# Kernel tuning notes

Hardware: AMD Instinct MI355X
Metric: run time of the kernel (lower is better)

## Reference

```python
import jax, jax.numpy as jnp
import numpy as np

DIM = 192
WINDOW = 8
HEADS = 6
N = WINDOW * WINDOW


def _relative_position_index(ws):
    coords = np.stack(np.meshgrid(np.arange(ws), np.arange(ws), indexing='ij'))  # (2, ws, ws)
    flat = coords.reshape(2, -1)  # (2, N)
    rel = flat[:, :, None] - flat[:, None, :]  # (2, N, N)
    rel = rel.transpose(1, 2, 0).copy()
    rel[:, :, 0] += ws - 1
    rel[:, :, 1] += ws - 1
    rel[:, :, 0] *= 2 * ws - 1
    return rel.sum(-1).astype(np.int32)  # (N, N)


def setup_inputs() -> dict:
    key = jax.random.key(0)
    ks = jax.random.split(key, 5)
    B_ = 4096
    x = jax.random.normal(ks[0], (B_, N, DIM), dtype=jnp.float32)
    qkv_w = jax.random.normal(ks[1], (3 * DIM, DIM), dtype=jnp.float32) * 0.02
    qkv_b = jnp.zeros((3 * DIM,), dtype=jnp.float32)
    proj_w = jax.random.normal(ks[2], (DIM, DIM), dtype=jnp.float32) * 0.02
    proj_b = jnp.zeros((DIM,), dtype=jnp.float32)
    rpb_table = jax.random.normal(ks[3], ((2 * WINDOW - 1) ** 2, HEADS), dtype=jnp.float32) * 0.02
    rel_idx = jnp.asarray(_relative_position_index(WINDOW))
    return {"x": x, "qkv_w": qkv_w, "qkv_b": qkv_b, "proj_w": proj_w,
            "proj_b": proj_b, "rpb_table": rpb_table, "rel_idx": rel_idx}


def reference(x, qkv_w, qkv_b, proj_w, proj_b, rpb_table, rel_idx):
    B_, n, C = x.shape
    d = C // HEADS
    scale = d ** -0.5
    qkv = x @ qkv_w.T + qkv_b                      # (B_, N, 3C)
    qkv = qkv.reshape(B_, n, 3, HEADS, d).transpose(2, 0, 3, 1, 4)  # (3, B_, H, N, d)
    q, k, v = qkv[0], qkv[1], qkv[2]
    attn = jnp.einsum('bhnd,bhmd->bhnm', q * scale, k)  # (B_, H, N, N)
    bias = rpb_table[rel_idx.reshape(-1)].reshape(n, n, HEADS).transpose(2, 0, 1)  # (H, N, N)
    attn = jax.nn.softmax(attn + bias[None], axis=-1)
    out = jnp.einsum('bhnm,bhmd->bnhd', attn, v).reshape(B_, n, C)
    return out @ proj_w.T + proj_b
```

## Files before the change

kernel.cpp:

```cpp
#include <hip/hip_runtime.h>


constexpr int NT = 64, DIMC = 192, NH = 6;
constexpr float SC = 0.17677669529663687f;

typedef short          s8v __attribute__((ext_vector_type(8)));
typedef float          f4v __attribute__((ext_vector_type(4)));
typedef unsigned short u4v __attribute__((ext_vector_type(4)));

constexpr size_t WS_QKVW  = 0;
constexpr size_t WS_PROJW = WS_QKVW + (size_t)36*6*2*1024;
constexpr size_t WS_BIAS  = WS_PROJW + (size_t)12*6*2*1024;
constexpr size_t WS_QKVB  = WS_BIAS + (size_t)6*4*4*64*16;
constexpr size_t WS_NEED  = WS_QKVB + (size_t)576*4;

__device__ __forceinline__ unsigned short bhi(float x) {
  return (unsigned short)(__builtin_bit_cast(unsigned int, x) >> 16);
}
__device__ __forceinline__ float bft(unsigned short h) {
  return __builtin_bit_cast(float, ((unsigned int)h) << 16);
}
__device__ __forceinline__ unsigned short brne(float x) {
  unsigned int u = __builtin_bit_cast(unsigned int, x);
  u += 0x7FFFu + ((u >> 16) & 1u);
  return (unsigned short)(u >> 16);
}

#define MFMA16(a, b, c) __builtin_amdgcn_mfma_f32_16x16x32_bf16((a), (b), (c), 0, 0, 0)

__device__ __forceinline__ s8v ld_frag(const unsigned short* base, int idx) {
  u4v a = *(const u4v*)(base + idx);
  u4v b = *(const u4v*)(base + idx + 16);
  s8v r;
  #pragma unroll
  for (int i = 0; i < 4; ++i) { r[i] = (short)a[i]; r[4 + i] = (short)b[i]; }
  return r;
}

__global__ __launch_bounds__(256) void prep_kernel(
    const float* __restrict__ qkv_w, const float* __restrict__ qkv_b,
    const float* __restrict__ proj_w, const float* __restrict__ rpb,
    const int* __restrict__ ridx, char* __restrict__ ws)
{
  const int t = blockIdx.x * 256 + threadIdx.x;
  if (t < 13824) {
    const int lane = t & 63, rest = t >> 6;
    const int kk = rest % 6, nt = rest / 6;
    const int g = lane >> 4, c = lane & 15;
    const int n = 16 * nt + c;
    const float sc = (nt < 12) ? SC : 1.f;
    const float* p = qkv_w + n * 192 + kk * 32 + 4 * g;
    f4v a = *(const f4v*)p;       a *= sc;
    f4v b = *(const f4v*)(p + 16); b *= sc;
    s8v hi, lo;
    #pragma unroll
    for (int i = 0; i < 4; ++i) {
      unsigned short h0 = bhi(a[i]); hi[i]     = (short)h0; lo[i]     = (short)brne(a[i] - bft(h0));
      unsigned short h1 = bhi(b[i]); hi[4 + i] = (short)h1; lo[4 + i] = (short)brne(b[i] - bft(h1));
    }
    s8v* base = (s8v*)(ws + WS_QKVW);
    base[((nt * 6 + kk) * 2 + 0) * 64 + lane] = hi;
    base[((nt * 6 + kk) * 2 + 1) * 64 + lane] = lo;
  } else if (t < 18432) {
    const int t2 = t - 13824;
    const int lane = t2 & 63, rest = t2 >> 6;
    const int h = rest % 6, nt = rest / 6;
    const int g = lane >> 4, c = lane & 15;
    const int n = 16 * nt + c;
    const float* p = proj_w + n * 192 + 32 * h + 4 * g;
    f4v a = *(const f4v*)p;
    f4v b = *(const f4v*)(p + 16);
    s8v hi, lo;
    #pragma unroll
    for (int i = 0; i < 4; ++i) {
      unsigned short h0 = bhi(a[i]); hi[i]     = (short)h0; lo[i]     = (short)brne(a[i] - bft(h0));
      unsigned short h1 = bhi(b[i]); hi[4 + i] = (short)h1; lo[4 + i] = (short)brne(b[i] - bft(h1));
    }
    s8v* base = (s8v*)(ws + WS_PROJW);
    base[((nt * 6 + h) * 2 + 0) * 64 + lane] = hi;
    base[((nt * 6 + h) * 2 + 1) * 64 + lane] = lo;
  } else if (t < 24576) {
    const int t2 = t - 18432;
    const int lane = t2 & 63, rest = t2 >> 6;
    const int nt = rest & 3, mt = (rest >> 2) & 3, h = rest >> 4;
    const int g = lane >> 4, c = lane & 15;
    const int q = 16 * nt + c;
    const int kb = 16 * mt + 4 * g;
    const int* ip = ridx + q * 64 + kb;
    f4v o;
    #pragma unroll
    for (int r = 0; r < 4; ++r) o[r] = rpb[ip[r] * 6 + h];
    ((f4v*)(ws + WS_BIAS))[((h * 4 + mt) * 4 + nt) * 64 + lane] = o;
  } else if (t < 25152) {
    const int i = t - 24576;
    ((float*)(ws + WS_QKVB))[i] = qkv_b[i] * (i < 192 ? SC : 1.f);
  }
}

__global__ __launch_bounds__(256, 2)
void win_attn_mfma(const float* __restrict__ x, const float* __restrict__ proj_b,
                   const char* __restrict__ ws, float* __restrict__ out)
{
  __shared__ alignas(16) unsigned short Qh[64 * 36], Ql[64 * 36];
  __shared__ alignas(16) unsigned short Kh[64 * 36], Kl[64 * 36];
  __shared__ alignas(16) unsigned short Vh[32 * 68], Vl[32 * 68];

  const int tid = threadIdx.x;
  const int wv = tid >> 6, lane = tid & 63, g = lane >> 4, c = lane & 15;
  const size_t win = blockIdx.x;
  const float* xw   = x   + win * (size_t)(NT * DIMC);
  float*       outw = out + win * (size_t)(NT * DIMC);

  const s8v*   qkvw  = (const s8v*)(ws + WS_QKVW);
  const s8v*   projw = (const s8v*)(ws + WS_PROJW);
  const f4v*   biasf = (const f4v*)(ws + WS_BIAS);
  const float* qkvb  = (const float*)(ws + WS_QKVB);

  f4v pacc[12];
  #pragma unroll
  for (int i = 0; i < 12; ++i)
    #pragma unroll
    for (int r = 0; r < 4; ++r) pacc[i][r] = 0.f;

  const float* xbase = xw + (size_t)(16 * wv + c) * DIMC + 4 * g;

  #pragma unroll 1
  for (int h = 0; h < NH; ++h) {
    f4v acc[6];
    #pragma unroll
    for (int j = 0; j < 6; ++j)
      #pragma unroll
      for (int r = 0; r < 4; ++r) acc[j][r] = 0.f;

    #pragma unroll
    for (int kk = 0; kk < 6; ++kk) {
      f4v xa = *(const f4v*)(xbase + 32 * kk);
      f4v xb = *(const f4v*)(xbase + 32 * kk + 16);
      s8v ah, al;
      #pragma unroll
      for (int i = 0; i < 4; ++i) {
        unsigned short h0 = bhi(xa[i]); ah[i]     = (short)h0; al[i]     = (short)brne(xa[i] - bft(h0));
        unsigned short h1 = bhi(xb[i]); ah[4 + i] = (short)h1; al[4 + i] = (short)brne(xb[i] - bft(h1));
      }
      #pragma unroll
      for (int sgj = 0; sgj < 6; ++sgj) {
        const int seg = sgj >> 1, j = sgj & 1;
        const int n576 = seg * 12 + 2 * h + j;
        const s8v bh = qkvw[((n576 * 6 + kk) * 2 + 0) * 64 + lane];
        const s8v bl = qkvw[((n576 * 6 + kk) * 2 + 1) * 64 + lane];
        acc[sgj] = MFMA16(ah, bh, acc[sgj]);
        acc[sgj] = MFMA16(ah, bl, acc[sgj]);
        acc[sgj] = MFMA16(al, bh, acc[sgj]);
      }
    }
    #pragma unroll
    for (int sgj = 0; sgj < 6; ++sgj) {
      const int seg = sgj >> 1, j = sgj & 1;
      const float bv = qkvb[seg * 192 + 32 * h + 16 * j + c];
      if (seg < 2) {
        unsigned short* dh = (seg == 0) ? Qh : Kh;
        unsigned short* dl = (seg == 0) ? Ql : Kl;
        #pragma unroll
        for (int r = 0; r < 4; ++r) {
          const float v = acc[sgj][r] + bv;
          const unsigned short hh = bhi(v);
          dh[(16 * wv + 4 * g + r) * 36 + 16 * j + c] = hh;
          dl[(16 * wv + 4 * g + r) * 36 + 16 * j + c] = brne(v - bft(hh));
        }
      } else {
        u4v hh, ll;
        #pragma unroll
        for (int r = 0; r < 4; ++r) {
          const float v = acc[sgj][r] + bv;
          const unsigned short x0 = bhi(v);
          hh[r] = x0; ll[r] = brne(v - bft(x0));
        }
        *(u4v*)&Vh[(16 * j + c) * 68 + 16 * wv + 4 * g] = hh;
        *(u4v*)&Vl[(16 * j + c) * 68 + 16 * wv + 4 * g] = ll;
      }
    }
    __syncthreads();

    f4v sacc[4];
    #pragma unroll
    for (int mt = 0; mt < 4; ++mt)
      sacc[mt] = biasf[((h * 4 + mt) * 4 + wv) * 64 + lane];

    s8v qbh, qbl;
    {
      const int idx = (16 * wv + c) * 36 + 4 * g;
      qbh = ld_frag(Qh, idx);
      qbl = ld_frag(Ql, idx);
    }
    #pragma unroll
    for (int mt = 0; mt < 4; ++mt) {
      const int idx = (16 * mt + c) * 36 + 4 * g;
      const s8v kh = ld_frag(Kh, idx);
      const s8v kl = ld_frag(Kl, idx);
      sacc[mt] = MFMA16(kh, qbh, sacc[mt]);
      sacc[mt] = MFMA16(kh, qbl, sacc[mt]);
      sacc[mt] = MFMA16(kl, qbh, sacc[mt]);
    }
    float mx = sacc[0][0];
    #pragma unroll
    for (int mt = 0; mt < 4; ++mt)
      #pragma unroll
      for (int r = 0; r < 4; ++r) mx = fmaxf(mx, sacc[mt][r]);
    mx = fmaxf(mx, __shfl_xor(mx, 16));
    mx = fmaxf(mx, __shfl_xor(mx, 32));
    float sum = 0.f;
    float p[4][4];
    #pragma unroll
    for (int mt = 0; mt < 4; ++mt)
      #pragma unroll
      for (int r = 0; r < 4; ++r) { p[mt][r] = __expf(sacc[mt][r] - mx); sum += p[mt][r]; }
    sum += __shfl_xor(sum, 16);
    sum += __shfl_xor(sum, 32);
    const float inv = 1.f / sum;
    unsigned short ph[4][4], pl[4][4];
    #pragma unroll
    for (int mt = 0; mt < 4; ++mt)
      #pragma unroll
      for (int r = 0; r < 4; ++r) {
        const float v = p[mt][r] * inv;
        const unsigned short h0 = bhi(v);
        ph[mt][r] = h0; pl[mt][r] = brne(v - bft(h0));
      }

    f4v oa0, oa1;
    #pragma unroll
    for (int r = 0; r < 4; ++r) { oa0[r] = 0.f; oa1[r] = 0.f; }
    #pragma unroll
    for (int kk = 0; kk < 2; ++kk) {
      s8v pbh, pbl;
      #pragma unroll
      for (int i = 0; i < 4; ++i) {
        pbh[i] = (short)ph[2 * kk][i];     pbl[i] = (short)pl[2 * kk][i];
        pbh[4 + i] = (short)ph[2 * kk + 1][i]; pbl[4 + i] = (short)pl[2 * kk + 1][i];
      }
      #pragma unroll
      for (int mo = 0; mo < 2; ++mo) {
        const int idx = (16 * mo + c) * 68 + 32 * kk + 4 * g;
        const s8v vh = ld_frag(Vh, idx);
        const s8v vl = ld_frag(Vl, idx);
        f4v& o = (mo == 0) ? oa0 : oa1;
        o = MFMA16(vh, pbh, o);
        o = MFMA16(vh, pbl, o);
        o = MFMA16(vl, pbh, o);
      }
    }
    __syncthreads();

    s8v oh, ol;
    #pragma unroll
    for (int i = 0; i < 4; ++i) {
      const unsigned short h0 = bhi(oa0[i]);
      oh[i] = (short)h0; ol[i] = (short)brne(oa0[i] - bft(h0));
      const unsigned short h1 = bhi(oa1[i]);
      oh[4 + i] = (short)h1; ol[4 + i] = (short)brne(oa1[i] - bft(h1));
    }
    #pragma unroll
    for (int nt = 0; nt < 12; ++nt) {
      const s8v wh = projw[((nt * 6 + h) * 2 + 0) * 64 + lane];
      const s8v wl = projw[((nt * 6 + h) * 2 + 1) * 64 + lane];
      pacc[nt] = MFMA16(oh, wh, pacc[nt]);
      pacc[nt] = MFMA16(oh, wl, pacc[nt]);
      pacc[nt] = MFMA16(ol, wh, pacc[nt]);
    }
  }

  #pragma unroll
  for (int nt = 0; nt < 12; ++nt) {
    const float pb = proj_b[16 * nt + c];
    #pragma unroll
    for (int r = 0; r < 4; ++r)
      outw[(size_t)(16 * wv + 4 * g + r) * DIMC + 16 * nt + c] = pacc[nt][r] + pb;
  }
}

__global__ __launch_bounds__(256, 2)
void win_attn_kernel(const float* __restrict__ x, const float* __restrict__ qkv_w,
                     const float* __restrict__ qkv_b, const float* __restrict__ proj_w,
                     const float* __restrict__ proj_b, const float* __restrict__ rpb,
                     const int* __restrict__ ridx, float* __restrict__ out)
{
  __shared__ float reg1[32 * 192];
  __shared__ float reg2[48 * 64];
  __shared__ float qs[64 * 36];
  __shared__ float ks[64 * 36];
  __shared__ float vs[64 * 36];

  const int tid = threadIdx.x;
  const int w = blockIdx.x;
  const float* xw = x + (size_t)w * (NT * DIMC);
  float* outw = out + (size_t)w * (NT * DIMC);

  const int cg = tid >> 4;
  const int tgA = tid & 15;
  const int tB = tid >> 2;
  const int jB = tid & 3;
  const int ogD = tid >> 4;
  const int tgD = tid & 15;

  int idxv[16];
  #pragma unroll
  for (int mm = 0; mm < 16; ++mm) idxv[mm] = ridx[tB * 64 + jB + 4 * mm] * NH;

  float oacc[4][12];
  #pragma unroll
  for (int tt = 0; tt < 4; ++tt)
    #pragma unroll
    for (int oo = 0; oo < 12; ++oo) oacc[tt][oo] = 0.f;

  for (int h = 0; h < NH; ++h) {
    float acc[6][4];
    #pragma unroll
    for (int cc = 0; cc < 6; ++cc)
      #pragma unroll
      for (int tt = 0; tt < 4; ++tt) acc[cc][tt] = 0.f;

    for (int i0 = 0; i0 < DIMC; i0 += 48) {
      __syncthreads();
      #pragma unroll
      for (int k = 0; k < 12; ++k) {
        int flat = k * 256 + tid;
        int t = flat & 63, ii = flat >> 6;
        reg2[ii * 64 + t] = xw[t * DIMC + i0 + ii];
      }
      #pragma unroll
      for (int k = 0; k < 18; ++k) {
        int flat = k * 256 + tid;
        int rr = flat % 96, ii = flat / 96;
        int seg = rr >> 5, lc = rr & 31;
        int grow = seg * 192 + h * 32 + lc;
        reg1[ii * 96 + rr] = qkv_w[grow * DIMC + i0 + ii];
      }
      __syncthreads();
      #pragma unroll 2
      for (int i = 0; i < 48; ++i) {
        float4 x4 = *(const float4*)(&reg2[i * 64 + 4 * tgA]);
        const float* wr = &reg1[i * 96 + 6 * cg];
        float2 w0 = *(const float2*)(wr + 0);
        float2 w1 = *(const float2*)(wr + 2);
        float2 w2 = *(const float2*)(wr + 4);
        float xa[4] = {x4.x, x4.y, x4.z, x4.w};
        float wa[6] = {w0.x, w0.y, w1.x, w1.y, w2.x, w2.y};
        #pragma unroll
        for (int cc = 0; cc < 6; ++cc)
          #pragma unroll
          for (int tt = 0; tt < 4; ++tt)
            acc[cc][tt] = fmaf(wa[cc], xa[tt], acc[cc][tt]);
      }
    }
    #pragma unroll
    for (int cc = 0; cc < 6; ++cc) {
      int cch = 6 * cg + cc;
      int seg = cch >> 5, lc = cch & 31;
      float bv = qkv_b[seg * 192 + h * 32 + lc];
      if (seg == 0) {
        #pragma unroll
        for (int tt = 0; tt < 4; ++tt)
          qs[(4 * tgA + tt) * 36 + lc] = (acc[cc][tt] + bv) * SC;
      } else if (seg == 1) {
        #pragma unroll
        for (int tt = 0; tt < 4; ++tt)
          ks[(4 * tgA + tt) * 36 + lc] = acc[cc][tt] + bv;
      } else {
        #pragma unroll
        for (int tt = 0; tt < 4; ++tt)
          vs[(4 * tgA + tt) * 36 + lc] = acc[cc][tt] + bv;
      }
    }
    __syncthreads();

    #pragma unroll
    for (int k = 0; k < 24; ++k) {
      int flat = k * 256 + tid;
      int o = flat % 192, ccc = flat / 192;
      reg1[ccc * 192 + o] = proj_w[o * DIMC + h * 32 + ccc];
    }

    float qr[32];
    {
      const float* qrow = &qs[tB * 36];
      #pragma unroll
      for (int d4 = 0; d4 < 8; ++d4) {
        float4 q4 = *(const float4*)(qrow + 4 * d4);
        qr[4*d4+0] = q4.x; qr[4*d4+1] = q4.y; qr[4*d4+2] = q4.z; qr[4*d4+3] = q4.w;
      }
    }
    float sv[16];
    #pragma unroll
    for (int mm = 0; mm < 16; ++mm) {
      const float* krow = &ks[(jB + 4 * mm) * 36];
      float a = rpb[idxv[mm] + h];
      #pragma unroll
      for (int d4 = 0; d4 < 8; ++d4) {
        float4 k4 = *(const float4*)(krow + 4 * d4);
        a = fmaf(qr[4*d4+0], k4.x, a);
        a = fmaf(qr[4*d4+1], k4.y, a);
        a = fmaf(qr[4*d4+2], k4.z, a);
        a = fmaf(qr[4*d4+3], k4.w, a);
      }
      sv[mm] = a;
    }
    float mx = sv[0];
    #pragma unroll
    for (int mm = 1; mm < 16; ++mm) mx = fmaxf(mx, sv[mm]);
    mx = fmaxf(mx, __shfl_xor(mx, 1));
    mx = fmaxf(mx, __shfl_xor(mx, 2));
    float sum = 0.f;
    #pragma unroll
    for (int mm = 0; mm < 16; ++mm) { sv[mm] = __expf(sv[mm] - mx); sum += sv[mm]; }
    sum += __shfl_xor(sum, 1);
    sum += __shfl_xor(sum, 2);
    const float inv = 1.f / sum;

    float part[32];
    #pragma unroll
    for (int dd = 0; dd < 32; ++dd) part[dd] = 0.f;
    #pragma unroll
    for (int mm = 0; mm < 16; ++mm) {
      float pv = sv[mm] * inv;
      const float* vrow = &vs[(jB + 4 * mm) * 36];
      #pragma unroll
      for (int d4 = 0; d4 < 8; ++d4) {
        float4 v4 = *(const float4*)(vrow + 4 * d4);
        part[4*d4+0] = fmaf(pv, v4.x, part[4*d4+0]);
        part[4*d4+1] = fmaf(pv, v4.y, part[4*d4+1]);
        part[4*d4+2] = fmaf(pv, v4.z, part[4*d4+2]);
        part[4*d4+3] = fmaf(pv, v4.w, part[4*d4+3]);
      }
    }
    float p16[16];
    {
      const bool hi2 = (jB & 1);
      #pragma unroll
      for (int k2 = 0; k2 < 16; ++k2) {
        float lo_v = part[k2], hi_v = part[16 + k2];
        float sendv = hi2 ? lo_v : hi_v;
        float keepv = hi2 ? hi_v : lo_v;
        float got = __shfl_xor(sendv, 1);
        p16[k2] = keepv + got;
      }
    }
    float p8[8];
    {
      const bool hi2 = (jB & 2);
      #pragma unroll
      for (int k2 = 0; k2 < 8; ++k2) {
        float lo_v = p16[k2], hi_v = p16[8 + k2];
        float sendv = hi2 ? lo_v : hi_v;
        float keepv = hi2 ? hi_v : lo_v;
        float got = __shfl_xor(sendv, 2);
        p8[k2] = keepv + got;
      }
    }
    const int dd0 = (jB & 1) * 16 + (jB & 2) * 4;
    #pragma unroll
    for (int k2 = 0; k2 < 8; ++k2)
      reg2[(dd0 + k2) * 64 + tB] = p8[k2];

    __syncthreads();

    {
      const int o0 = 12 * ogD, t0 = 4 * tgD;
      #pragma unroll 2
      for (int cc2 = 0; cc2 < 32; ++cc2) {
        float4 a4 = *(const float4*)(&reg2[cc2 * 64 + t0]);
        const float* pr = &reg1[cc2 * 192 + o0];
        float4 b0 = *(const float4*)(pr + 0);
        float4 b1 = *(const float4*)(pr + 4);
        float4 b2 = *(const float4*)(pr + 8);
        float av[4]  = {a4.x, a4.y, a4.z, a4.w};
        float bw[12] = {b0.x, b0.y, b0.z, b0.w, b1.x, b1.y, b1.z, b1.w,
                        b2.x, b2.y, b2.z, b2.w};
        #pragma unroll
        for (int tt = 0; tt < 4; ++tt)
          #pragma unroll
          for (int oo = 0; oo < 12; ++oo)
            oacc[tt][oo] = fmaf(av[tt], bw[oo], oacc[tt][oo]);
      }
    }
  }

  {
    const int o0 = 12 * ogD, t0 = 4 * tgD;
    #pragma unroll
    for (int oo = 0; oo < 12; ++oo) {
      float pb = proj_b[o0 + oo];
      #pragma unroll
      for (int tt = 0; tt < 4; ++tt)
        outw[(size_t)(t0 + tt) * DIMC + o0 + oo] = oacc[tt][oo] + pb;
    }
  }
}

extern "C" void kernel_launch(void* const* d_in, const int* in_sizes, int n_in,
                              void* d_out, int out_size, void* d_ws, size_t ws_size,
                              hipStream_t stream) {
  const float* x      = (const float*)d_in[0];
  const float* qkv_w  = (const float*)d_in[1];
  const float* qkv_b  = (const float*)d_in[2];
  const float* proj_w = (const float*)d_in[3];
  const float* proj_b = (const float*)d_in[4];
  const float* rpb    = (const float*)d_in[5];
  const int*   ridx   = (const int*)d_in[6];
  float* out = (float*)d_out;
  const int B = in_sizes[0] / (NT * DIMC);

  if (d_ws != nullptr && ws_size >= WS_NEED) {
    hipLaunchKernelGGL(prep_kernel, dim3(99), dim3(256), 0, stream,
                       qkv_w, qkv_b, proj_w, rpb, ridx, (char*)d_ws);
    hipLaunchKernelGGL(win_attn_mfma, dim3(B), dim3(256), 0, stream,
                       x, proj_b, (const char*)d_ws, out);
  } else {
    hipLaunchKernelGGL(win_attn_kernel, dim3(B), dim3(256), 0, stream,
                       x, qkv_w, qkv_b, proj_w, proj_b, rpb, ridx, out);
  }
}
```

Before: 1.035 ms.

## Double-buffer per-head QKV in LDS and overlap next head's projection with attention

Restructures the per-head loop into a software pipeline: Q/K/V LDS buffers are doubled, and the QKV projection MFMAs for head h+1 are issued between the QK^T and softmax/PV of head h, with the output projection of head h-1 deferred into the next iteration. This removes one of the two barriers per head and aims to hide MFMA and global-load latency behind softmax work. Softmax normalisation is also moved after PV (scaling the output by 1/sum instead of scaling the probabilities). LDS use doubles and register pressure rises from the extra live accumulators, which may hurt occupancy at the 2-block launch bound.

```diff
diff --git a/kernel.cpp b/kernel.cpp
--- a/kernel.cpp
+++ b/kernel.cpp
@@ -97,13 +97,183 @@
   }
 }
 
+
+__device__ __forceinline__ void qkv_head(int lane, const float* __restrict__ xbase,
+                                         const s8v* __restrict__ qkvw,
+                                         int h, f4v acc[6]) {
+  #pragma unroll
+  for (int j = 0; j < 6; ++j)
+    #pragma unroll
+    for (int r = 0; r < 4; ++r) acc[j][r] = 0.f;
+  #pragma unroll
+  for (int kk = 0; kk < 6; ++kk) {
+    f4v xa = *(const f4v*)(xbase + 32 * kk);
+    f4v xb = *(const f4v*)(xbase + 32 * kk + 16);
+    s8v ah, al;
+    #pragma unroll
+    for (int i = 0; i < 4; ++i) {
+      unsigned short h0 = bhi(xa[i]); ah[i]     = (short)h0; al[i]     = (short)brne(xa[i] - bft(h0));
+      unsigned short h1 = bhi(xb[i]); ah[4 + i] = (short)h1; al[4 + i] = (short)brne(xb[i] - bft(h1));
+    }
+    #pragma unroll
+    for (int sgj = 0; sgj < 6; ++sgj) {
+      const int seg = sgj >> 1, j = sgj & 1;
+      const int n576 = seg * 12 + 2 * h + j;
+      const s8v bh = qkvw[((n576 * 6 + kk) * 2 + 0) * 64 + lane];
+      const s8v bl = qkvw[((n576 * 6 + kk) * 2 + 1) * 64 + lane];
+      acc[sgj] = MFMA16(ah, bh, acc[sgj]);
+      acc[sgj] = MFMA16(ah, bl, acc[sgj]);
+      acc[sgj] = MFMA16(al, bh, acc[sgj]);
+    }
+  }
+}
+
+__device__ __forceinline__ void qkv_stage(int wv, int g, int c,
+    const f4v acc[6], const float* __restrict__ qkvb, int h,
+    unsigned short* Qh_, unsigned short* Ql_,
+    unsigned short* Kh_, unsigned short* Kl_,
+    unsigned short* Vh_, unsigned short* Vl_) {
+  #pragma unroll
+  for (int sgj = 0; sgj < 6; ++sgj) {
+    const int seg = sgj >> 1, j = sgj & 1;
+    const float bv = qkvb[seg * 192 + 32 * h + 16 * j + c];
+    if (seg < 2) {
+      unsigned short* dh = (seg == 0) ? Qh_ : Kh_;
+      unsigned short* dl = (seg == 0) ? Ql_ : Kl_;
+      #pragma unroll
+      for (int r = 0; r < 4; ++r) {
+        const float v = acc[sgj][r] + bv;
+        const unsigned short hh = bhi(v);
+        dh[(16 * wv + 4 * g + r) * 36 + 16 * j + c] = hh;
+        dl[(16 * wv + 4 * g + r) * 36 + 16 * j + c] = brne(v - bft(hh));
+      }
+    } else {
+      u4v hh, ll;
+      #pragma unroll
+      for (int r = 0; r < 4; ++r) {
+        const float v = acc[sgj][r] + bv;
+        const unsigned short x0 = bhi(v);
+        hh[r] = x0; ll[r] = brne(v - bft(x0));
+      }
+      *(u4v*)&Vh_[(16 * j + c) * 68 + 16 * wv + 4 * g] = hh;
+      *(u4v*)&Vl_[(16 * j + c) * 68 + 16 * wv + 4 * g] = ll;
+    }
+  }
+}
+
+__device__ __forceinline__ void proj_acc(int lane, const s8v oh, const s8v ol,
+                                         const s8v* __restrict__ projw, int h,
+                                         f4v pacc[12]) {
+  #pragma unroll
+  for (int nt = 0; nt < 12; ++nt) {
+    const s8v wh = projw[((nt * 6 + h) * 2 + 0) * 64 + lane];
+    const s8v wl = projw[((nt * 6 + h) * 2 + 1) * 64 + lane];
+    pacc[nt] = MFMA16(oh, wh, pacc[nt]);
+    pacc[nt] = MFMA16(oh, wl, pacc[nt]);
+    pacc[nt] = MFMA16(ol, wh, pacc[nt]);
+  }
+}
+
+template<bool DO_NEXT>
+__device__ __forceinline__ void head_iter(
+    int h, int lane, int wv, int g, int c,
+    const float* __restrict__ xbase,
+    const s8v* __restrict__ qkvw, const f4v* __restrict__ biasf,
+    const float* __restrict__ qkvb,
+    const unsigned short* Qhc, const unsigned short* Qlc,
+    const unsigned short* Khc, const unsigned short* Klc,
+    const unsigned short* Vhc, const unsigned short* Vlc,
+    unsigned short* Qhn, unsigned short* Qln,
+    unsigned short* Khn, unsigned short* Kln,
+    unsigned short* Vhn, unsigned short* Vln,
+    s8v& oh, s8v& ol)
+{
+  f4v sacc[4];
+  #pragma unroll
+  for (int mt = 0; mt < 4; ++mt)
+    sacc[mt] = biasf[((h * 4 + mt) * 4 + wv) * 64 + lane];
+  s8v qbh, qbl;
+  {
+    const int idx = (16 * wv + c) * 36 + 4 * g;
+    qbh = ld_frag(Qhc, idx);
+    qbl = ld_frag(Qlc, idx);
+  }
+  #pragma unroll
+  for (int mt = 0; mt < 4; ++mt) {
+    const int idx = (16 * mt + c) * 36 + 4 * g;
+    const s8v kh = ld_frag(Khc, idx);
+    const s8v kl = ld_frag(Klc, idx);
+    sacc[mt] = MFMA16(kh, qbh, sacc[mt]);
+    sacc[mt] = MFMA16(kh, qbl, sacc[mt]);
+    sacc[mt] = MFMA16(kl, qbh, sacc[mt]);
+  }
+
+  f4v acc2[6];
+  if (DO_NEXT) qkv_head(lane, xbase, qkvw, h + 1, acc2);
+
+  float mx = sacc[0][0];
+  #pragma unroll
+  for (int mt = 0; mt < 4; ++mt)
+    #pragma unroll
+    for (int r = 0; r < 4; ++r) mx = fmaxf(mx, sacc[mt][r]);
+  mx = fmaxf(mx, __shfl_xor(mx, 16));
+  mx = fmaxf(mx, __shfl_xor(mx, 32));
+  float pv[4][4];
+  float sum = 0.f;
+  #pragma unroll
+  for (int mt = 0; mt < 4; ++mt)
+    #pragma unroll
+    for (int r = 0; r < 4; ++r) { pv[mt][r] = __expf(sacc[mt][r] - mx); sum += pv[mt][r]; }
+
+  f4v oa0, oa1;
+  #pragma unroll
+  for (int r = 0; r < 4; ++r) { oa0[r] = 0.f; oa1[r] = 0.f; }
+  #pragma unroll
+  for (int kk = 0; kk < 2; ++kk) {
+    s8v pbh, pbl;
+    #pragma unroll
+    for (int i = 0; i < 4; ++i) {
+      const float v0 = pv[2 * kk][i];
+      const float v1 = pv[2 * kk + 1][i];
+      const unsigned short h0 = bhi(v0), h1 = bhi(v1);
+      pbh[i]     = (short)h0; pbl[i]     = (short)brne(v0 - bft(h0));
+      pbh[4 + i] = (short)h1; pbl[4 + i] = (short)brne(v1 - bft(h1));
+    }
+    #pragma unroll
+    for (int mo = 0; mo < 2; ++mo) {
+      const int idx = (16 * mo + c) * 68 + 32 * kk + 4 * g;
+      const s8v vh = ld_frag(Vhc, idx);
+      const s8v vl = ld_frag(Vlc, idx);
+      f4v& o = (mo == 0) ? oa0 : oa1;
+      o = MFMA16(vh, pbh, o);
+      o = MFMA16(vh, pbl, o);
+      o = MFMA16(vl, pbh, o);
+    }
+  }
+  sum += __shfl_xor(sum, 16);
+  sum += __shfl_xor(sum, 32);
+  const float inv = 1.f / sum;
+
+  #pragma unroll
+  for (int i = 0; i < 4; ++i) {
+    const float v0 = oa0[i] * inv;
+    const unsigned short h0 = bhi(v0);
+    oh[i] = (short)h0; ol[i] = (short)brne(v0 - bft(h0));
+    const float v1 = oa1[i] * inv;
+    const unsigned short h1 = bhi(v1);
+    oh[4 + i] = (short)h1; ol[4 + i] = (short)brne(v1 - bft(h1));
+  }
+
+  if (DO_NEXT) qkv_stage(wv, g, c, acc2, qkvb, h + 1, Qhn, Qln, Khn, Kln, Vhn, Vln);
+}
+
 __global__ __launch_bounds__(256, 2)
 void win_attn_mfma(const float* __restrict__ x, const float* __restrict__ proj_b,
                    const char* __restrict__ ws, float* __restrict__ out)
 {
-  __shared__ alignas(16) unsigned short Qh[64 * 36], Ql[64 * 36];
-  __shared__ alignas(16) unsigned short Kh[64 * 36], Kl[64 * 36];
-  __shared__ alignas(16) unsigned short Vh[32 * 68], Vl[32 * 68];
+  __shared__ alignas(16) unsigned short QhS[2][64 * 36], QlS[2][64 * 36];
+  __shared__ alignas(16) unsigned short KhS[2][64 * 36], KlS[2][64 * 36];
+  __shared__ alignas(16) unsigned short VhS[2][32 * 68], VlS[2][32 * 68];
 
   const int tid = threadIdx.x;
   const int wv = tid >> 6, lane = tid & 63, g = lane >> 4, c = lane & 15;
@@ -124,150 +294,40 @@
 
   const float* xbase = xw + (size_t)(16 * wv + c) * DIMC + 4 * g;
 
+  {
+    f4v acc0[6];
+    qkv_head(lane, xbase, qkvw, 0, acc0);
+    qkv_stage(wv, g, c, acc0, qkvb, 0,
+              QhS[0], QlS[0], KhS[0], KlS[0], VhS[0], VlS[0]);
+  }
+  __syncthreads();
+
+  s8v oh{}, ol{};
+
+  head_iter<true>(0, lane, wv, g, c, xbase, qkvw, biasf, qkvb,
+                  QhS[0], QlS[0], KhS[0], KlS[0], VhS[0], VlS[0],
+                  QhS[1], QlS[1], KhS[1], KlS[1], VhS[1], VlS[1],
+                  oh, ol);
+  __syncthreads();
+
   #pragma unroll 1
-  for (int h = 0; h < NH; ++h) {
-    f4v acc[6];
-    #pragma unroll
-    for (int j = 0; j < 6; ++j)
-      #pragma unroll
-      for (int r = 0; r < 4; ++r) acc[j][r] = 0.f;
-
-    #pragma unroll
-    for (int kk = 0; kk < 6; ++kk) {
-      f4v xa = *(const f4v*)(xbase + 32 * kk);
-      f4v xb = *(const f4v*)(xbase + 32 * kk + 16);
-      s8v ah, al;
-      #pragma unroll
-      for (int i = 0; i < 4; ++i) {
-        unsigned short h0 = bhi(xa[i]); ah[i]     = (short)h0; al[i]     = (short)brne(xa[i] - bft(h0));
-        unsigned short h1 = bhi(xb[i]); ah[4 + i] = (short)h1; al[4 + i] = (short)brne(xb[i] - bft(h1));
-      }
-      #pragma unroll
-      for (int sgj = 0; sgj < 6; ++sgj) {
-        const int seg = sgj >> 1, j = sgj & 1;
-        const int n576 = seg * 12 + 2 * h + j;
-        const s8v bh = qkvw[((n576 * 6 + kk) * 2 + 0) * 64 + lane];
-        const s8v bl = qkvw[((n576 * 6 + kk) * 2 + 1) * 64 + lane];
-        acc[sgj] = MFMA16(ah, bh, acc[sgj]);
-        acc[sgj] = MFMA16(ah, bl, acc[sgj]);
-        acc[sgj] = MFMA16(al, bh, acc[sgj]);
-      }
-    }
-    #pragma unroll
-    for (int sgj = 0; sgj < 6; ++sgj) {
-      const int seg = sgj >> 1, j = sgj & 1;
-      const float bv = qkvb[seg * 192 + 32 * h + 16 * j + c];
-      if (seg < 2) {
-        unsigned short* dh = (seg == 0) ? Qh : Kh;
-        unsigned short* dl = (seg == 0) ? Ql : Kl;
-        #pragma unroll
-        for (int r = 0; r < 4; ++r) {
-          const float v = acc[sgj][r] + bv;
-          const unsigned short hh = bhi(v);
-          dh[(16 * wv + 4 * g + r) * 36 + 16 * j + c] = hh;
-          dl[(16 * wv + 4 * g + r) * 36 + 16 * j + c] = brne(v - bft(hh));
-        }
-      } else {
-        u4v hh, ll;
-        #pragma unroll
-        for (int r = 0; r < 4; ++r) {
-          const float v = acc[sgj][r] + bv;
-          const unsigned short x0 = bhi(v);
-          hh[r] = x0; ll[r] = brne(v - bft(x0));
-        }
-        *(u4v*)&Vh[(16 * j + c) * 68 + 16 * wv + 4 * g] = hh;
-        *(u4v*)&Vl[(16 * j + c) * 68 + 16 * wv + 4 * g] = ll;
-      }
-    }
+  for (int h = 1; h < NH - 1; ++h) {
+    const int p = h & 1;
+    proj_acc(lane, oh, ol, projw, h - 1, pacc);
+    head_iter<true>(h, lane, wv, g, c, xbase, qkvw, biasf, qkvb,
+                    QhS[p], QlS[p], KhS[p], KlS[p], VhS[p], VlS[p],
+                    QhS[p ^ 1], QlS[p ^ 1], KhS[p ^ 1], KlS[p ^ 1],
+                    VhS[p ^ 1], VlS[p ^ 1],
+                    oh, ol);
     __syncthreads();
-
-    f4v sacc[4];
-    #pragma unroll
-    for (int mt = 0; mt < 4; ++mt)
-      sacc[mt] = biasf[((h * 4 + mt) * 4 + wv) * 64 + lane];
-
-    s8v qbh, qbl;
-    {
-      const int idx = (16 * wv + c) * 36 + 4 * g;
-      qbh = ld_frag(Qh, idx);
-      qbl = ld_frag(Ql, idx);
-    }
-    #pragma unroll
-    for (int mt = 0; mt < 4; ++mt) {
-      const int idx = (16 * mt + c) * 36 + 4 * g;
-      const s8v kh = ld_frag(Kh, idx);
-      const s8v kl = ld_frag(Kl, idx);
-      sacc[mt] = MFMA16(kh, qbh, sacc[mt]);
-      sacc[mt] = MFMA16(kh, qbl, sacc[mt]);
-      sacc[mt] = MFMA16(kl, qbh, sacc[mt]);
-    }
-    float mx = sacc[0][0];
-    #pragma unroll
-    for (int mt = 0; mt < 4; ++mt)
-      #pragma unroll
-      for (int r = 0; r < 4; ++r) mx = fmaxf(mx, sacc[mt][r]);
-    mx = fmaxf(mx, __shfl_xor(mx, 16));
-    mx = fmaxf(mx, __shfl_xor(mx, 32));
-    float sum = 0.f;
-    float p[4][4];
-    #pragma unroll
-    for (int mt = 0; mt < 4; ++mt)
-      #pragma unroll
-      for (int r = 0; r < 4; ++r) { p[mt][r] = __expf(sacc[mt][r] - mx); sum += p[mt][r]; }
-    sum += __shfl_xor(sum, 16);
-    sum += __shfl_xor(sum, 32);
-    const float inv = 1.f / sum;
-    unsigned short ph[4][4], pl[4][4];
-    #pragma unroll
-    for (int mt = 0; mt < 4; ++mt)
-      #pragma unroll
-      for (int r = 0; r < 4; ++r) {
-        const float v = p[mt][r] * inv;
-        const unsigned short h0 = bhi(v);
-        ph[mt][r] = h0; pl[mt][r] = brne(v - bft(h0));
-      }
-
-    f4v oa0, oa1;
-    #pragma unroll
-    for (int r = 0; r < 4; ++r) { oa0[r] = 0.f; oa1[r] = 0.f; }
-    #pragma unroll
-    for (int kk = 0; kk < 2; ++kk) {
-      s8v pbh, pbl;
-      #pragma unroll
-      for (int i = 0; i < 4; ++i) {
-        pbh[i] = (short)ph[2 * kk][i];     pbl[i] = (short)pl[2 * kk][i];
-        pbh[4 + i] = (short)ph[2 * kk + 1][i]; pbl[4 + i] = (short)pl[2 * kk + 1][i];
-      }
-      #pragma unroll
-      for (int mo = 0; mo < 2; ++mo) {
-        const int idx = (16 * mo + c) * 68 + 32 * kk + 4 * g;
-        const s8v vh = ld_frag(Vh, idx);
-        const s8v vl = ld_frag(Vl, idx);
-        f4v& o = (mo == 0) ? oa0 : oa1;
-        o = MFMA16(vh, pbh, o);
-        o = MFMA16(vh, pbl, o);
-        o = MFMA16(vl, pbh, o);
-      }
-    }
-    __syncthreads();
-
-    s8v oh, ol;
-    #pragma unroll
-    for (int i = 0; i < 4; ++i) {
-      const unsigned short h0 = bhi(oa0[i]);
-      oh[i] = (short)h0; ol[i] = (short)brne(oa0[i] - bft(h0));
-      const unsigned short h1 = bhi(oa1[i]);
-      oh[4 + i] = (short)h1; ol[4 + i] = (short)brne(oa1[i] - bft(h1));
-    }
-    #pragma unroll
-    for (int nt = 0; nt < 12; ++nt) {
-      const s8v wh = projw[((nt * 6 + h) * 2 + 0) * 64 + lane];
-      const s8v wl = projw[((nt * 6 + h) * 2 + 1) * 64 + lane];
-      pacc[nt] = MFMA16(oh, wh, pacc[nt]);
-      pacc[nt] = MFMA16(oh, wl, pacc[nt]);
-      pacc[nt] = MFMA16(ol, wh, pacc[nt]);
-    }
-  }
+  }
+
+  proj_acc(lane, oh, ol, projw, 4, pacc);
+  head_iter<false>(5, lane, wv, g, c, xbase, qkvw, biasf, qkvb,
+                   QhS[1], QlS[1], KhS[1], KlS[1], VhS[1], VlS[1],
+                   QhS[0], QlS[0], KhS[0], KlS[0], VhS[0], VlS[0],
+                   oh, ol);
+  proj_acc(lane, oh, ol, projw, 5, pacc);
 
   #pragma unroll
   for (int nt = 0; nt < 12; ++nt) {
@@ -421,15 +481,15 @@
     for (int dd = 0; dd < 32; ++dd) part[dd] = 0.f;
     #pragma unroll
     for (int mm = 0; mm < 16; ++mm) {
-      float pv = sv[mm] * inv;
+      float pvv = sv[mm] * inv;
       const float* vrow = &vs[(jB + 4 * mm) * 36];
       #pragma unroll
       for (int d4 = 0; d4 < 8; ++d4) {
         float4 v4 = *(const float4*)(vrow + 4 * d4);
-        part[4*d4+0] = fmaf(pv, v4.x, part[4*d4+0]);
-        part[4*d4+1] = fmaf(pv, v4.y, part[4*d4+1]);
-        part[4*d4+2] = fmaf(pv, v4.z, part[4*d4+2]);
-        part[4*d4+3] = fmaf(pv, v4.w, part[4*d4+3]);
+        part[4*d4+0] = fmaf(pvv, v4.x, part[4*d4+0]);
+        part[4*d4+1] = fmaf(pvv, v4.y, part[4*d4+1]);
+        part[4*d4+2] = fmaf(pvv, v4.z, part[4*d4+2]);
+        part[4*d4+3] = fmaf(pvv, v4.w, part[4*d4+3]);
       }
     }
     float p16[16];
```

Result: faster. 937.4 us (-9.4%).
